# Performance work log

Hardware: AMD Instinct MI355X
Metric: run time of the kernel (lower is better)

## Reference

```python
import jax, jax.numpy as jnp
import numpy as np

B, V, E, L = 1024, 50000, 256, 17  # batch, nodeNum(vocab), embeddingSize, Huffman path length


def setup_inputs() -> dict:
    key = jax.random.key(0)
    k1, k2, k3, k4, k5 = jax.random.split(key, 5)
    x = jax.random.normal(k1, (B, V), dtype=jnp.float32)
    W = jax.random.normal(k2, (E, V), dtype=jnp.float32) * 0.02  # nn.Linear(nodeNum, embeddingSize).weight
    b = jax.random.normal(k3, (E,), dtype=jnp.float32) * 0.02    # nn.Linear bias
    path_vectors = jax.random.normal(k4, (B, L, E), dtype=jnp.float32)  # gathered treeNode.vector along each target's path
    path_signs = jax.random.randint(k5, (B, L), 0, 2, dtype=jnp.int32)  # 1 == 'left' (+v), 0 == 'right' (-v)
    return {"x": x, "W": W, "b": b, "path_vectors": path_vectors, "path_signs": path_signs}


def reference(x, W, b, path_vectors, path_signs):
    # x = self.embeddingSpace(x)
    emb = x @ W.T + b  # [B, E]
    # direct == 'left' -> +node.vector, 'right' -> -node.vector
    signs = (2 * path_signs - 1).astype(emb.dtype)  # [B, L] in {-1, +1}
    logits = jnp.einsum('ble,be->bl', path_vectors, emb) * signs  # per-node dot
    # output = prod_over_path sigmoid(dot)
    return jnp.prod(jax.nn.sigmoid(logits), axis=-1)  # [B]
```

## Files before the change

### kernel.cpp

```cpp
#include <hip/hip_runtime.h>
#include <hip/hip_bf16.h>
#include <math.h>

#define VDIM 50000
#define BDIM 1024
#define EDIM 256
#define LDIM 17

constexpr int BM = 128, BN = 128, BK = 32;
constexpr int KT_FULL = VDIM / BK;
constexpr int SPLITS  = 64;
constexpr int TAILZ   = KT_FULL % SPLITS;
constexpr int NBLK    = (EDIM / BN) * (BDIM / BM) * SPLITS;

typedef _Float16 f16x8 __attribute__((ext_vector_type(8)));
typedef float    f32x4 __attribute__((ext_vector_type(4)));

__device__ __forceinline__ void async_f4(const float* g, float* l) {
    __builtin_amdgcn_global_load_lds(
        (const __attribute__((address_space(1))) void*)g,
        (__attribute__((address_space(3))) void*)l, 16, 0, 0);
}

__device__ __forceinline__ f16x8 cvt8(const float4 f0, const float4 f1) {
    f16x8 r;
    r[0] = (_Float16)f0.x; r[1] = (_Float16)f0.y;
    r[2] = (_Float16)f0.z; r[3] = (_Float16)f0.w;
    r[4] = (_Float16)f1.x; r[5] = (_Float16)f1.y;
    r[6] = (_Float16)f1.z; r[7] = (_Float16)f1.w;
    return r;
}

__global__ __launch_bounds__(256, 4) void gemm_f16(
    const float* __restrict__ X, const float* __restrict__ Wm,
    float* __restrict__ wsout, const int part) {
    __shared__ __align__(16) float sA[BM * BK];
    __shared__ __align__(16) float sB[BN * BK];

    const int tid = threadIdx.x;

    const int n   = blockIdx.x;
    const int r   = n & 7;
    const int q   = n >> 3;
    const int z   = (r << 3) + (q >> 4);
    const int t16 = q & 15;
    const int bn0 = (t16 & 1) * BN;
    const int bm0 = (t16 >> 1) * BM;

    const int lane = tid & 63;
    const int wv   = tid >> 6;
    const int wm0  = (wv >> 1) * 64;
    const int wn0  = (wv & 1) * 64;
    const int lm   = lane & 15;
    const int gk0  = (lane >> 4) * 2;

    const int rsub   = lane >> 3;
    const int grp    = lane & 7;
    const int coloff = ((grp ^ rsub) << 2);
    const int rowS   = wv * 32 + rsub;

    f32x4 acc[4][4] = {};

    auto issue = [&](int kt) {
        const int k0 = kt * BK;
#pragma unroll
        for (int j = 0; j < 4; ++j) {
            const int row = rowS + j * 8;
            async_f4(X  + (size_t)(bm0 + row) * VDIM + k0 + coloff, &sA[(wv * 32 + j * 8) * BK]);
            async_f4(Wm + (size_t)(bn0 + row) * VDIM + k0 + coloff, &sB[(wv * 32 + j * 8) * BK]);
        }
    };

    auto compute = [&]() {
        const float* A  = sA;
        const float* Bs = sB;
        f16x8 ah[4];
#pragma unroll
        for (int mi = 0; mi < 4; ++mi) {
            const int row = wm0 + mi * 16 + lm;
            const int s = row & 7;
            const float4 f0 = *reinterpret_cast<const float4*>(&A[row * BK + ((gk0 ^ s) << 2)]);
            const float4 f1 = *reinterpret_cast<const float4*>(&A[row * BK + (((gk0 + 1) ^ s) << 2)]);
            ah[mi] = cvt8(f0, f1);
        }
#pragma unroll
        for (int ni = 0; ni < 4; ++ni) {
            const int row = wn0 + ni * 16 + lm;
            const int s = row & 7;
            const float4 f0 = *reinterpret_cast<const float4*>(&Bs[row * BK + ((gk0 ^ s) << 2)]);
            const float4 f1 = *reinterpret_cast<const float4*>(&Bs[row * BK + (((gk0 + 1) ^ s) << 2)]);
            const f16x8 bh = cvt8(f0, f1);
            __builtin_amdgcn_s_setprio(1);
#pragma unroll
            for (int mi = 0; mi < 4; ++mi)
                acc[mi][ni] = __builtin_amdgcn_mfma_f32_16x16x32_f16(ah[mi], bh, acc[mi][ni], 0, 0, 0);
            __builtin_amdgcn_s_setprio(0);
        }
    };

    for (int kt = z; kt < KT_FULL; kt += SPLITS) {
        __syncthreads();
        issue(kt);
        __syncthreads();
        compute();
    }

    if (z == TAILZ) {
        const int k0 = KT_FULL * BK;
        __syncthreads();
#pragma unroll
        for (int j = 0; j < 4; ++j) {
            const int row = rowS + j * 8;
            float4 va = make_float4(0.f, 0.f, 0.f, 0.f), vb = va;
            if (coloff < 16) {
                va = *reinterpret_cast<const float4*>(X  + (size_t)(bm0 + row) * VDIM + k0 + coloff);
                vb = *reinterpret_cast<const float4*>(Wm + (size_t)(bn0 + row) * VDIM + k0 + coloff);
            }
            *reinterpret_cast<float4*>(&sA[row * BK + (grp << 2)]) = va;
            *reinterpret_cast<float4*>(&sB[row * BK + (grp << 2)]) = vb;
        }
        __syncthreads();
        compute();
    }

    const int orow = (lane >> 4) * 4;
    if (part) {
        float* dst = wsout + (size_t)z * BDIM * EDIM;
#pragma unroll
        for (int mi = 0; mi < 4; ++mi)
#pragma unroll
            for (int ni = 0; ni < 4; ++ni)
#pragma unroll
                for (int r2 = 0; r2 < 4; ++r2) {
                    const int gm = bm0 + wm0 + mi * 16 + orow + r2;
                    const int gn = bn0 + wn0 + ni * 16 + lm;
                    dst[(size_t)gm * EDIM + gn] = acc[mi][ni][r2];
                }
    } else {
#pragma unroll
        for (int mi = 0; mi < 4; ++mi)
#pragma unroll
            for (int ni = 0; ni < 4; ++ni)
#pragma unroll
                for (int r2 = 0; r2 < 4; ++r2) {
                    const int gm = bm0 + wm0 + mi * 16 + orow + r2;
                    const int gn = bn0 + wn0 + ni * 16 + lm;
                    atomicAdd(&wsout[gm * EDIM + gn], acc[mi][ni][r2]);
                }
    }
}

__global__ __launch_bounds__(256) void stage2_kernel(
    const float* __restrict__ ws, const float* __restrict__ bias,
    const float* __restrict__ pv, const int* __restrict__ signs,
    float* __restrict__ out, const int part) {
    const int b = blockIdx.x;
    __shared__ float se[EDIM];
    __shared__ float wp[4];
    const int t = threadIdx.x;
    float s = bias[t];
    if (part) {
#pragma unroll
        for (int zz = 0; zz < SPLITS; ++zz)
            s += ws[((size_t)zz * BDIM + b) * EDIM + t];
    } else {
        s += ws[b * EDIM + t];
    }
    se[t] = s;
    __syncthreads();
    const int w = t >> 6, lane = t & 63;
    float p = 1.0f;
    for (int l = w; l < LDIM; l += 4) {
        const float4 a = *reinterpret_cast<const float4*>(&pv[((size_t)b * LDIM + l) * EDIM + lane * 4]);
        const float4 e = *reinterpret_cast<const float4*>(&se[lane * 4]);
        float d = a.x * e.x + a.y * e.y + a.z * e.z + a.w * e.w;
#pragma unroll
        for (int off = 32; off > 0; off >>= 1) d += __shfl_xor(d, off, 64);
        const float zz = signs[b * LDIM + l] ? d : -d;
        p *= 1.0f / (1.0f + expf(-zz));
    }
    if (lane == 0) wp[w] = p;
    __syncthreads();
    if (t == 0) out[b] = wp[0] * wp[1] * wp[2] * wp[3];
}

extern "C" void kernel_launch(void* const* d_in, const int* in_sizes, int n_in,
                              void* d_out, int out_size, void* d_ws, size_t ws_size,
                              hipStream_t stream) {
    const float* X    = (const float*)d_in[0];
    const float* Wm   = (const float*)d_in[1];
    const float* bias = (const float*)d_in[2];
    const float* pv   = (const float*)d_in[3];
    const int*   sg   = (const int*)d_in[4];
    float* out = (float*)d_out;
    float* ws  = (float*)d_ws;

    const size_t need = (size_t)SPLITS * BDIM * EDIM * sizeof(float);
    const int part = (ws_size >= need) ? 1 : 0;

    if (!part)
        hipMemsetAsync(ws, 0, (size_t)BDIM * EDIM * sizeof(float), stream);

    gemm_f16<<<dim3(NBLK), 256, 0, stream>>>(X, Wm, ws, part);

    stage2_kernel<<<BDIM, 256, 0, stream>>>(ws, bias, pv, sg, out, part);
}
```

Before: 397.3 us.

## Enlarge GEMM tiles to 256x256 with 1024 threads and double-buffered LDS

Tiles grow to 256x256, so each block covers the full embedding width with 16 waves, and the grid shrinks to 256 blocks. Waves 0-7 stage X and waves 8-15 stage W. Each X row is now fetched once instead of twice, and W is fetched half as often, which cuts global traffic on a memory-bound split-K GEMM. The LDS buffers are double-buffered so async loads for the next K-slice overlap the MFMA work on the current one, with one barrier per iteration. The cost is about 128KB of LDS per block, so only one block fits per CU, and fewer blocks are left to hide latency.

```diff
diff --git a/kernel.cpp b/kernel.cpp
--- a/kernel.cpp
+++ b/kernel.cpp
@@ -7,7 +7,7 @@
 #define EDIM 256
 #define LDIM 17
 
-constexpr int BM = 128, BN = 128, BK = 32;
+constexpr int BM = 256, BN = 256, BK = 32;
 constexpr int KT_FULL = VDIM / BK;
 constexpr int SPLITS  = 64;
 constexpr int TAILZ   = KT_FULL % SPLITS;
@@ -31,49 +31,55 @@
     return r;
 }
 
-__global__ __launch_bounds__(256, 4) void gemm_f16(
+__global__ __launch_bounds__(1024, 4) void gemm_f16(
     const float* __restrict__ X, const float* __restrict__ Wm,
     float* __restrict__ wsout, const int part) {
-    __shared__ __align__(16) float sA[BM * BK];
-    __shared__ __align__(16) float sB[BN * BK];
+    __shared__ __align__(16) float sA[2][BM * BK];
+    __shared__ __align__(16) float sB[2][BN * BK];
 
     const int tid = threadIdx.x;
 
     const int n   = blockIdx.x;
     const int r   = n & 7;
     const int q   = n >> 3;
-    const int z   = (r << 3) + (q >> 4);
-    const int t16 = q & 15;
-    const int bn0 = (t16 & 1) * BN;
-    const int bm0 = (t16 >> 1) * BM;
+    const int z   = (r << 3) + (q >> 2);
+    const int bm0 = (q & 3) * BM;
+    const int bn0 = 0;
 
     const int lane = tid & 63;
     const int wv   = tid >> 6;
-    const int wm0  = (wv >> 1) * 64;
-    const int wn0  = (wv & 1) * 64;
+    const int wm0  = (wv >> 2) * 64;
+    const int wn0  = (wv & 3) * 64;
     const int lm   = lane & 15;
     const int gk0  = (lane >> 4) * 2;
 
     const int rsub   = lane >> 3;
     const int grp    = lane & 7;
     const int coloff = ((grp ^ rsub) << 2);
-    const int rowS   = wv * 32 + rsub;
+    const int stg    = (wv & 7) * 32;
 
     f32x4 acc[4][4] = {};
 
-    auto issue = [&](int kt) {
+    auto issue = [&](int kt, int pb) {
         const int k0 = kt * BK;
-#pragma unroll
-        for (int j = 0; j < 4; ++j) {
-            const int row = rowS + j * 8;
-            async_f4(X  + (size_t)(bm0 + row) * VDIM + k0 + coloff, &sA[(wv * 32 + j * 8) * BK]);
-            async_f4(Wm + (size_t)(bn0 + row) * VDIM + k0 + coloff, &sB[(wv * 32 + j * 8) * BK]);
+        if (wv < 8) {
+#pragma unroll
+            for (int j = 0; j < 4; ++j) {
+                const int row = stg + j * 8 + rsub;
+                async_f4(X + (size_t)(bm0 + row) * VDIM + k0 + coloff, &sA[pb][(stg + j * 8) * BK]);
+            }
+        } else {
+#pragma unroll
+            for (int j = 0; j < 4; ++j) {
+                const int row = stg + j * 8 + rsub;
+                async_f4(Wm + (size_t)(bn0 + row) * VDIM + k0 + coloff, &sB[pb][(stg + j * 8) * BK]);
+            }
         }
     };
 
-    auto compute = [&]() {
-        const float* A  = sA;
-        const float* Bs = sB;
+    auto compute = [&](int pb) {
+        const float* A  = sA[pb];
+        const float* Bs = sB[pb];
         f16x8 ah[4];
 #pragma unroll
         for (int mi = 0; mi < 4; ++mi) {
@@ -98,29 +104,33 @@
         }
     };
 
-    for (int kt = z; kt < KT_FULL; kt += SPLITS) {
+    int pb = 0;
+    issue(z, 0);
+    for (int kt = z + SPLITS; kt < KT_FULL; kt += SPLITS) {
         __syncthreads();
-        issue(kt);
-        __syncthreads();
-        compute();
-    }
+        issue(kt, pb ^ 1);
+        compute(pb);
+        pb ^= 1;
+    }
+    __syncthreads();
+    compute(pb);
 
     if (z == TAILZ) {
         const int k0 = KT_FULL * BK;
         __syncthreads();
 #pragma unroll
         for (int j = 0; j < 4; ++j) {
-            const int row = rowS + j * 8;
-            float4 va = make_float4(0.f, 0.f, 0.f, 0.f), vb = va;
-            if (coloff < 16) {
-                va = *reinterpret_cast<const float4*>(X  + (size_t)(bm0 + row) * VDIM + k0 + coloff);
-                vb = *reinterpret_cast<const float4*>(Wm + (size_t)(bn0 + row) * VDIM + k0 + coloff);
-            }
-            *reinterpret_cast<float4*>(&sA[row * BK + (grp << 2)]) = va;
-            *reinterpret_cast<float4*>(&sB[row * BK + (grp << 2)]) = vb;
+            const int row = stg + j * 8 + rsub;
+            float4 v = make_float4(0.f, 0.f, 0.f, 0.f);
+            if (coloff < 16)
+                v = *reinterpret_cast<const float4*>(
+                        (wv < 8 ? X + (size_t)(bm0 + row) * VDIM : Wm + (size_t)(bn0 + row) * VDIM)
+                        + k0 + coloff);
+            float* dstl = (wv < 8 ? &sA[pb ^ 1][0] : &sB[pb ^ 1][0]);
+            *reinterpret_cast<float4*>(&dstl[row * BK + (grp << 2)]) = v;
         }
         __syncthreads();
-        compute();
+        compute(pb ^ 1);
     }
 
     const int orow = (lane >> 4) * 4;
@@ -201,7 +211,7 @@
     if (!part)
         hipMemsetAsync(ws, 0, (size_t)BDIM * EDIM * sizeof(float), stream);
 
-    gemm_f16<<<dim3(NBLK), 256, 0, stream>>>(X, Wm, ws, part);
+    gemm_f16<<<dim3(NBLK), 1024, 0, stream>>>(X, Wm, ws, part);
 
     stage2_kernel<<<BDIM, 256, 0, stream>>>(ws, bias, pv, sg, out, part);
 }
```

Result: faster. 385.6 us (-3.0%).
